# Kernel tuning notes

Hardware: AMD Instinct MI355X
Metric: run time of the kernel (lower is better)

Reference implementation:

```python
import jax, jax.numpy as jnp
import numpy as np

N_NODES = 100000
N_EDGES = 1600000
D_IN, D_HID, D_OUT = 64, 64, 32


def setup_inputs() -> dict:
    key = jax.random.key(0)
    ks = jax.random.split(key, 9)
    x = jax.random.normal(ks[0], (N_NODES, D_IN), dtype=jnp.float32)
    edge_index = jax.random.randint(ks[1], (2, N_EDGES), 0, N_NODES, dtype=jnp.int64)
    s1 = 1.0 / np.sqrt(D_IN)
    s2 = 1.0 / np.sqrt(D_HID)
    return {
        "x": x,
        "edge_index": edge_index,
        # layer 1: lin_l (aggregated neighbors, has bias), lin_r (root, no bias)
        "W1_l": jax.random.uniform(ks[2], (D_IN, D_HID), jnp.float32, -s1, s1),
        "b1": jax.random.uniform(ks[3], (D_HID,), jnp.float32, -s1, s1),
        "W1_r": jax.random.uniform(ks[4], (D_IN, D_HID), jnp.float32, -s1, s1),
        # layer 2
        "W2_l": jax.random.uniform(ks[5], (D_HID, D_OUT), jnp.float32, -s2, s2),
        "b2": jax.random.uniform(ks[6], (D_OUT,), jnp.float32, -s2, s2),
        "W2_r": jax.random.uniform(ks[7], (D_HID, D_OUT), jnp.float32, -s2, s2),
    }


def _sage_conv(x, src, dst, W_l, b_l, W_r, n_nodes):
    """PyG SAGEConv with mean aggregation:
       out_i = W_l @ mean_{j in N(i)} x_j + b_l + W_r @ x_i
    """
    msgs = x[src]  # [E, d] gather of source-node features
    summed = jax.ops.segment_sum(msgs, dst, num_segments=n_nodes)  # [N, d]
    deg = jax.ops.segment_sum(jnp.ones((src.shape[0],), x.dtype), dst, num_segments=n_nodes)
    mean = summed / jnp.maximum(deg, 1.0)[:, None]
    return mean @ W_l + b_l + x @ W_r


def reference(x, edge_index, W1_l, b1, W1_r, W2_l, b2, W2_r):
    src, dst = edge_index[0], edge_index[1]
    n = x.shape[0]
    h = _sage_conv(x, src, dst, W1_l, b1, W1_r, n)
    h = jax.nn.relu(h)
    out = _sage_conv(h, src, dst, W2_l, b2, W2_r, n)
    return out
```

## Files before the change

### kernel.cpp

```cpp
#include <hip/hip_runtime.h>


typedef __attribute__((ext_vector_type(4))) float f4;
typedef __attribute__((ext_vector_type(2))) float f2;
typedef __attribute__((ext_vector_type(4))) unsigned short us4;
typedef __attribute__((ext_vector_type(8))) unsigned short us8;
typedef __attribute__((ext_vector_type(8))) short bfrag;

#define BSHIFT 9
#define BSZ (1 << BSHIFT)
#define NBMAX 256
#define NBLK 512
#define LSTR 72

static __device__ inline unsigned short f2bf(float f) {
    union { float f; unsigned u; } v; v.f = f;
    unsigned u = v.u;
    u = (u + 0x7FFFu + ((u >> 16) & 1u)) >> 16;
    return (unsigned short)u;
}
static __device__ inline float bf2f(unsigned short h) {
    union { unsigned u; float f; } v; v.u = ((unsigned)h) << 16; return v.f;
}

__global__ __launch_bounds__(256) void k_bhist(const int* __restrict__ dst, int E, int chunk,
                                               int NB, int* __restrict__ cntmat) {
    __shared__ int hist[NBMAX];
    int t = threadIdx.x;
    hist[t] = 0;
    __syncthreads();
    int lo = blockIdx.x * chunk, hi = min(lo + chunk, E);
    for (int e = lo + t; e < hi; e += 256) atomicAdd(&hist[dst[e] >> BSHIFT], 1);
    __syncthreads();
    if (t < NB) cntmat[blockIdx.x * NB + t] = hist[t];
}

__global__ __launch_bounds__(256) void k_cscan(int* __restrict__ cntmat, int NB,
                                               int* __restrict__ btot) {
    __shared__ int wt[4];
    int b = blockIdx.x;
    int t = threadIdx.x;
    int v0 = cntmat[(2 * t) * NB + b];
    int v1 = cntmat[(2 * t + 1) * NB + b];
    int tsum = v0 + v1;
    int lane = t & 63, w = t >> 6;
    int p = tsum;
    for (int off = 1; off < 64; off <<= 1) { int u = __shfl_up(p, off); if (lane >= off) p += u; }
    if (lane == 63) wt[w] = p;
    __syncthreads();
    int wb = 0;
    for (int i = 0; i < w; i++) wb += wt[i];
    int excl = wb + p - tsum;
    cntmat[(2 * t) * NB + b] = excl;
    cntmat[(2 * t + 1) * NB + b] = excl + v0;
    if (t == 255) btot[b] = wb + p;
}

__global__ __launch_bounds__(256) void k_bscan(const int* __restrict__ btot, int NB, int E, int N,
                                               int* __restrict__ bucket_base,
                                               int* __restrict__ row_off) {
    __shared__ int wt[4];
    int t = threadIdx.x;
    int v = (t < NB) ? btot[t] : 0;
    int lane = t & 63, w = t >> 6;
    int p = v;
    for (int off = 1; off < 64; off <<= 1) { int u = __shfl_up(p, off); if (lane >= off) p += u; }
    if (lane == 63) wt[w] = p;
    __syncthreads();
    int wb = 0;
    for (int i = 0; i < w; i++) wb += wt[i];
    int incl = wb + p;
    int excl = incl - v;
    if (t < NB) bucket_base[t] = excl;
    if (t == NB - 1) bucket_base[NB] = incl;
    if (t == 0) row_off[N] = E;
}

__global__ __launch_bounds__(256) void k_bscatter(const int* __restrict__ src, const int* __restrict__ dst,
                                                  int E, int chunk, int NB,
                                                  const int* __restrict__ bucket_base,
                                                  const int* __restrict__ cntmat,
                                                  unsigned int* __restrict__ bdata) {
    __shared__ int lbase[NBMAX], lcur[NBMAX];
    int t = threadIdx.x;
    if (t < NB) { lbase[t] = bucket_base[t] + cntmat[blockIdx.x * NB + t]; lcur[t] = 0; }
    __syncthreads();
    int lo = blockIdx.x * chunk, hi = min(lo + chunk, E);
    for (int e = lo + t; e < hi; e += 256) {
        int d = dst[e];
        int b = d >> BSHIFT;
        int pos = lbase[b] + atomicAdd(&lcur[b], 1);
        bdata[pos] = ((unsigned)(d & (BSZ - 1)) << 17) | (unsigned)src[e];
    }
}

__global__ __launch_bounds__(256) void k_bucket_csr(const unsigned int* __restrict__ bdata,
                                                    const int* __restrict__ bucket_base,
                                                    int N, int* __restrict__ row_off,
                                                    int* __restrict__ col_src) {
    __shared__ int fh[BSZ];
    __shared__ int wtot[4];
    int t = threadIdx.x;
    int b = blockIdx.x;
    int ebase = bucket_base[b], eend = bucket_base[b + 1];
    fh[2 * t] = 0; fh[2 * t + 1] = 0;
    __syncthreads();
    for (int i = ebase + t; i < eend; i += 256) atomicAdd(&fh[bdata[i] >> 17], 1);
    __syncthreads();
    int a0 = fh[2 * t], a1 = fh[2 * t + 1];
    int psum = a0 + a1;
    int lane = t & 63, w = t >> 6;
    int v = psum;
    for (int off = 1; off < 64; off <<= 1) { int u = __shfl_up(v, off); if (lane >= off) v += u; }
    if (lane == 63) wtot[w] = v;
    __syncthreads();
    int wbase = 0;
    for (int i = 0; i < w; i++) wbase += wtot[i];
    int excl = wbase + v - psum;
    int e0 = excl, e1 = excl + a0;
    int n0 = (b << BSHIFT) + 2 * t, n1 = n0 + 1;
    if (n0 < N) row_off[n0] = ebase + e0;
    if (n1 < N) row_off[n1] = ebase + e1;
    fh[2 * t] = e0; fh[2 * t + 1] = e1;
    __syncthreads();
    for (int i = ebase + t; i < eend; i += 256) {
        unsigned vv = bdata[i];
        int dl = vv >> 17;
        int pos = atomicAdd(&fh[dl], 1);
        col_src[ebase + pos] = (int)(vv & 0x1FFFFu);
    }
}

__global__ __launch_bounds__(256) void k_gemm1(const float* __restrict__ x,
                                               const float* __restrict__ Wl,
                                               const float* __restrict__ Wr, int N,
                                               unsigned char* __restrict__ t1l8,
                                               float* __restrict__ t1r) {
    __shared__ unsigned short sX[64 * LSTR];
    __shared__ unsigned short sW[128 * LSTR];
    int t = threadIdx.x;
    int r0 = blockIdx.x * 64;
    for (int i = t; i < 2048; i += 256) {
        int which = i >> 10;
        int rem = i & 1023;
        int k = rem >> 4;
        int c4 = (rem & 15) * 4;
        f4 v = *(const f4*)&(which ? Wr : Wl)[k * 64 + c4];
        int nb = which * 64 + c4;
        sW[(nb + 0) * LSTR + k] = f2bf(v[0]);
        sW[(nb + 1) * LSTR + k] = f2bf(v[1]);
        sW[(nb + 2) * LSTR + k] = f2bf(v[2]);
        sW[(nb + 3) * LSTR + k] = f2bf(v[3]);
    }
    {
        int row = t >> 2;
        int q = (t & 3) * 16;
        bool valid = (r0 + row) < N;
#pragma unroll
        for (int j = 0; j < 4; j++) {
            f4 v = {0.f, 0.f, 0.f, 0.f};
            if (valid) v = *(const f4*)&x[(size_t)(r0 + row) * 64 + q + j * 4];
            us4 bv;
            bv[0] = f2bf(v[0]); bv[1] = f2bf(v[1]); bv[2] = f2bf(v[2]); bv[3] = f2bf(v[3]);
            *(us4*)&sX[row * LSTR + q + j * 4] = bv;
        }
    }
    __syncthreads();
    int wv = t >> 6;
    int l  = t & 63;
    int lm = l & 15;
    int lk = (l >> 4) * 8;
    f4 acc[8] = {{0.f,0.f,0.f,0.f},{0.f,0.f,0.f,0.f},{0.f,0.f,0.f,0.f},{0.f,0.f,0.f,0.f},
                 {0.f,0.f,0.f,0.f},{0.f,0.f,0.f,0.f},{0.f,0.f,0.f,0.f},{0.f,0.f,0.f,0.f}};
#pragma unroll
    for (int kh = 0; kh < 2; kh++) {
        bfrag a = *(const bfrag*)&sX[(wv * 16 + lm) * LSTR + kh * 32 + lk];
#pragma unroll
        for (int nt = 0; nt < 8; nt++) {
            bfrag b = *(const bfrag*)&sW[(nt * 16 + lm) * LSTR + kh * 32 + lk];
            acc[nt] = __builtin_amdgcn_mfma_f32_16x16x32_bf16(a, b, acc[nt], 0, 0, 0);
        }
    }
    int orow0 = r0 + wv * 16 + (l >> 4) * 4;
#pragma unroll
    for (int j = 0; j < 4; j++) {
        int rr = orow0 + j;
        if (rr < N) {
#pragma unroll
            for (int nt = 0; nt < 4; nt++) {
                float v = acc[nt][j];
                unsigned w8 = __builtin_amdgcn_cvt_pk_fp8_f32(v, v, 0u, false);
                t1l8[(size_t)rr * 64 + nt * 16 + lm] = (unsigned char)(w8 & 0xFFu);
            }
#pragma unroll
            for (int nt = 0; nt < 4; nt++) {
                t1r[(size_t)rr * 64 + nt * 16 + lm] = acc[nt + 4][j];
            }
        }
    }
}

__global__ __launch_bounds__(256) void k_gemm2(const unsigned short* __restrict__ hbf,
                                               const float* __restrict__ Wl,
                                               const float* __restrict__ Wr,
                                               const float* __restrict__ b2, int N,
                                               unsigned short* __restrict__ t2l,
                                               float* __restrict__ t2r) {
    __shared__ unsigned short sX[64 * LSTR];
    __shared__ unsigned short sW[64 * LSTR];
    int t = threadIdx.x;
    int r0 = blockIdx.x * 64;
    for (int i = t; i < 1024; i += 256) {
        int which = i >> 9;
        int rem = i & 511;
        int k = rem >> 3;
        int c4 = (rem & 7) * 4;
        f4 v = *(const f4*)&(which ? Wr : Wl)[k * 32 + c4];
        int nb = which * 32 + c4;
        sW[(nb + 0) * LSTR + k] = f2bf(v[0]);
        sW[(nb + 1) * LSTR + k] = f2bf(v[1]);
        sW[(nb + 2) * LSTR + k] = f2bf(v[2]);
        sW[(nb + 3) * LSTR + k] = f2bf(v[3]);
    }
    {
        int row = t >> 2;
        int q = (t & 3) * 16;
        us8 z = {0,0,0,0,0,0,0,0};
        us8 v0 = z, v1 = z;
        if (r0 + row < N) {
            v0 = *(const us8*)&hbf[(size_t)(r0 + row) * 64 + q];
            v1 = *(const us8*)&hbf[(size_t)(r0 + row) * 64 + q + 8];
        }
        *(us8*)&sX[row * LSTR + q] = v0;
        *(us8*)&sX[row * LSTR + q + 8] = v1;
    }
    __syncthreads();
    int wv = t >> 6;
    int l  = t & 63;
    int lm = l & 15;
    int lk = (l >> 4) * 8;
    f4 acc[4] = {{0.f,0.f,0.f,0.f},{0.f,0.f,0.f,0.f},{0.f,0.f,0.f,0.f},{0.f,0.f,0.f,0.f}};
#pragma unroll
    for (int kh = 0; kh < 2; kh++) {
        bfrag a = *(const bfrag*)&sX[(wv * 16 + lm) * LSTR + kh * 32 + lk];
#pragma unroll
        for (int nt = 0; nt < 4; nt++) {
            bfrag b = *(const bfrag*)&sW[(nt * 16 + lm) * LSTR + kh * 32 + lk];
            acc[nt] = __builtin_amdgcn_mfma_f32_16x16x32_bf16(a, b, acc[nt], 0, 0, 0);
        }
    }
    int orow0 = r0 + wv * 16 + (l >> 4) * 4;
#pragma unroll
    for (int j = 0; j < 4; j++) {
        int rr = orow0 + j;
        if (rr < N) {
#pragma unroll
            for (int nt = 0; nt < 2; nt++) {
                t2l[(size_t)rr * 32 + nt * 16 + lm] = f2bf(acc[nt][j]);
            }
#pragma unroll
            for (int nt = 0; nt < 2; nt++) {
                int c = nt * 16 + lm;
                t2r[(size_t)rr * 32 + c] = acc[nt + 2][j] + b2[c];
            }
        }
    }
}

__global__ __launch_bounds__(256) void k_agg1(const unsigned char* __restrict__ t1l8,
                                              const int* __restrict__ row_off,
                                              const int* __restrict__ col_src,
                                              const float* __restrict__ b1,
                                              const float* __restrict__ t1r,
                                              int N, unsigned short* __restrict__ hbf) {
    int gid = (blockIdx.x * blockDim.x + threadIdx.x) >> 4;
    int gl  = threadIdx.x & 15;
    if (gid >= N) return;
    int beg = row_off[gid], end = row_off[gid + 1];
    f4 a0 = {0.f,0.f,0.f,0.f}, a1 = {0.f,0.f,0.f,0.f};
    f4 a2 = {0.f,0.f,0.f,0.f}, a3 = {0.f,0.f,0.f,0.f};
    int k = beg;
    for (; k + 3 < end; k += 4) {
        int i0 = col_src[k], i1 = col_src[k + 1], i2 = col_src[k + 2], i3 = col_src[k + 3];
        unsigned u0 = *(const unsigned*)&t1l8[(size_t)i0 * 64 + gl * 4];
        unsigned u1 = *(const unsigned*)&t1l8[(size_t)i1 * 64 + gl * 4];
        unsigned u2 = *(const unsigned*)&t1l8[(size_t)i2 * 64 + gl * 4];
        unsigned u3 = *(const unsigned*)&t1l8[(size_t)i3 * 64 + gl * 4];
        f2 l0 = __builtin_amdgcn_cvt_pk_f32_fp8(u0, false), h0 = __builtin_amdgcn_cvt_pk_f32_fp8(u0, true);
        f2 l1 = __builtin_amdgcn_cvt_pk_f32_fp8(u1, false), h1 = __builtin_amdgcn_cvt_pk_f32_fp8(u1, true);
        f2 l2 = __builtin_amdgcn_cvt_pk_f32_fp8(u2, false), h2 = __builtin_amdgcn_cvt_pk_f32_fp8(u2, true);
        f2 l3 = __builtin_amdgcn_cvt_pk_f32_fp8(u3, false), h3 = __builtin_amdgcn_cvt_pk_f32_fp8(u3, true);
        a0[0] += l0[0]; a0[1] += l0[1]; a0[2] += h0[0]; a0[3] += h0[1];
        a1[0] += l1[0]; a1[1] += l1[1]; a1[2] += h1[0]; a1[3] += h1[1];
        a2[0] += l2[0]; a2[1] += l2[1]; a2[2] += h2[0]; a2[3] += h2[1];
        a3[0] += l3[0]; a3[1] += l3[1]; a3[2] += h3[0]; a3[3] += h3[1];
    }
    for (; k < end; k++) {
        unsigned u0 = *(const unsigned*)&t1l8[(size_t)col_src[k] * 64 + gl * 4];
        f2 l0 = __builtin_amdgcn_cvt_pk_f32_fp8(u0, false), h0 = __builtin_amdgcn_cvt_pk_f32_fp8(u0, true);
        a0[0] += l0[0]; a0[1] += l0[1]; a0[2] += h0[0]; a0[3] += h0[1];
    }
    f4 s = (a0 + a1) + (a2 + a3);
    float deg = (float)(end - beg);
    float inv = deg > 0.f ? 1.f / deg : 0.f;
    f4 rr = *(const f4*)&t1r[(size_t)gid * 64 + gl * 4];
    f4 bb = *(const f4*)&b1[gl * 4];
    us4 ob;
#pragma unroll
    for (int j = 0; j < 4; j++) {
        float v = s[j] * inv + rr[j] + bb[j];
        ob[j] = f2bf(v > 0.f ? v : 0.f);
    }
    *(us4*)&hbf[(size_t)gid * 64 + gl * 4] = ob;
}

__global__ __launch_bounds__(256) void k_agg2(const unsigned short* __restrict__ t2l,
                                              const float* __restrict__ t2r,
                                              const int* __restrict__ row_off,
                                              const int* __restrict__ col_src,
                                              int N, float* __restrict__ out) {
    int gid = (blockIdx.x * blockDim.x + threadIdx.x) >> 4;
    int gl  = threadIdx.x & 15;
    if (gid >= N) return;
    int beg = row_off[gid], end = row_off[gid + 1];
    f2 a0 = {0.f,0.f}, a1 = {0.f,0.f}, a2 = {0.f,0.f}, a3 = {0.f,0.f};
    int k = beg;
    for (; k + 3 < end; k += 4) {
        int i0 = col_src[k], i1 = col_src[k + 1], i2 = col_src[k + 2], i3 = col_src[k + 3];
        unsigned u0 = *(const unsigned*)&t2l[(size_t)i0 * 32 + gl * 2];
        unsigned u1 = *(const unsigned*)&t2l[(size_t)i1 * 32 + gl * 2];
        unsigned u2 = *(const unsigned*)&t2l[(size_t)i2 * 32 + gl * 2];
        unsigned u3 = *(const unsigned*)&t2l[(size_t)i3 * 32 + gl * 2];
        a0[0] += bf2f((unsigned short)(u0 & 0xFFFFu)); a0[1] += bf2f((unsigned short)(u0 >> 16));
        a1[0] += bf2f((unsigned short)(u1 & 0xFFFFu)); a1[1] += bf2f((unsigned short)(u1 >> 16));
        a2[0] += bf2f((unsigned short)(u2 & 0xFFFFu)); a2[1] += bf2f((unsigned short)(u2 >> 16));
        a3[0] += bf2f((unsigned short)(u3 & 0xFFFFu)); a3[1] += bf2f((unsigned short)(u3 >> 16));
    }
    for (; k < end; k++) {
        unsigned u0 = *(const unsigned*)&t2l[(size_t)col_src[k] * 32 + gl * 2];
        a0[0] += bf2f((unsigned short)(u0 & 0xFFFFu)); a0[1] += bf2f((unsigned short)(u0 >> 16));
    }
    f2 s = (a0 + a1) + (a2 + a3);
    float deg = (float)(end - beg);
    float inv = deg > 0.f ? 1.f / deg : 0.f;
    f2 rr = *(const f2*)&t2r[(size_t)gid * 32 + gl * 2];
    f2 o = {s[0] * inv + rr[0], s[1] * inv + rr[1]};
    *(f2*)&out[(size_t)gid * 32 + gl * 2] = o;
}

extern "C" void kernel_launch(void* const* d_in, const int* in_sizes, int n_in,
                              void* d_out, int out_size, void* d_ws, size_t ws_size,
                              hipStream_t stream) {
    const float* x   = (const float*)d_in[0];
    const int*   ei  = (const int*)d_in[1];
    const float* W1l = (const float*)d_in[2];
    const float* b1  = (const float*)d_in[3];
    const float* W1r = (const float*)d_in[4];
    const float* W2l = (const float*)d_in[5];
    const float* b2  = (const float*)d_in[6];
    const float* W2r = (const float*)d_in[7];
    float* out = (float*)d_out;

    int N = in_sizes[0] / 64;
    int E = in_sizes[1] / 2;
    const int* src = ei;
    const int* dst = ei + E;
    int NB = (N + BSZ - 1) >> BSHIFT;

    char* ws = (char*)d_ws;
    size_t off = 0;
    auto alloc = [&](size_t bytes) { void* p = ws + off; off += (bytes + 255) & ~(size_t)255; return p; };
    int* cntmat      = (int*)alloc((size_t)NBLK * NB * 4);
    int* btot        = (int*)alloc((size_t)NB * 4);
    int* bucket_base = (int*)alloc((size_t)(NB + 1) * 4);
    int* row_off     = (int*)alloc((size_t)(N + 1) * 4);
    int* col_src     = (int*)alloc((size_t)E * 4);
    unsigned int* bdata = (unsigned int*)alloc((size_t)E * 4);
    unsigned char* t1l8 = (unsigned char*)alloc((size_t)N * 64);
    float* t1r          = (float*)alloc((size_t)N * 64 * 4);
    unsigned short* hbf = (unsigned short*)alloc((size_t)N * 64 * 2);

    unsigned short* t2l = (unsigned short*)bdata;
    float* t2r          = t1r;

    int chunk = (E + NBLK - 1) / NBLK;
    k_bhist<<<NBLK, 256, 0, stream>>>(dst, E, chunk, NB, cntmat);
    k_cscan<<<NB, 256, 0, stream>>>(cntmat, NB, btot);
    k_bscan<<<1, 256, 0, stream>>>(btot, NB, E, N, bucket_base, row_off);
    k_bscatter<<<NBLK, 256, 0, stream>>>(src, dst, E, chunk, NB, bucket_base, cntmat, bdata);
    k_bucket_csr<<<NB, 256, 0, stream>>>(bdata, bucket_base, N, row_off, col_src);

    int gb = (N + 63) / 64;
    k_gemm1<<<gb, 256, 0, stream>>>(x, W1l, W1r, N, t1l8, t1r);
    k_agg1<<<((size_t)N * 16 + 255) / 256, 256, 0, stream>>>(t1l8, row_off, col_src, b1, t1r, N, hbf);
    k_gemm2<<<gb, 256, 0, stream>>>(hbf, W2l, W2r, b2, N, t2l, t2r);
    k_agg2<<<((size_t)N * 16 + 255) / 256, 256, 0, stream>>>(t2l, t2r, row_off, col_src, N, out);
}
```

Before: 142.2 us.

## Split gather tables into feature planes, fold bucket scan, store root term bf16

The gathered neighbor tables for both layers are split into two column planes: layer 1 fp8 as 32-byte rows, layer 2 bf16 as 32-byte rows. Each aggregation kernel is launched twice, once per plane, so each pass gathers from a table half the size and is more likely to stay cache-resident. The single-block bucket scan kernel is removed; its prefix sum is recomputed redundantly inside the scatter and CSR kernels, saving one launch. The layer-1 root term is stored as bf16 instead of fp32, halving that traffic at some precision cost, but the CSR indices and row offsets are now read twice per layer.

```diff
diff --git a/kernel.cpp b/kernel.cpp
--- a/kernel.cpp
+++ b/kernel.cpp
@@ -35,8 +35,8 @@
     if (t < NB) cntmat[blockIdx.x * NB + t] = hist[t];
 }
 
-__global__ __launch_bounds__(256) void k_cscan(int* __restrict__ cntmat, int NB,
-                                               int* __restrict__ btot) {
+__global__ __launch_bounds__(256) void k_cscan(int* __restrict__ cntmat, int NB, int E, int N,
+                                               int* __restrict__ btot, int* __restrict__ row_off) {
     __shared__ int wt[4];
     int b = blockIdx.x;
     int t = threadIdx.x;
@@ -54,11 +54,15 @@
     cntmat[(2 * t) * NB + b] = excl;
     cntmat[(2 * t + 1) * NB + b] = excl + v0;
     if (t == 255) btot[b] = wb + p;
-}
-
-__global__ __launch_bounds__(256) void k_bscan(const int* __restrict__ btot, int NB, int E, int N,
-                                               int* __restrict__ bucket_base,
-                                               int* __restrict__ row_off) {
+    if (b == 0 && t == 0) row_off[N] = E;
+}
+
+__global__ __launch_bounds__(256) void k_bscatter(const int* __restrict__ src, const int* __restrict__ dst,
+                                                  int E, int chunk, int NB,
+                                                  const int* __restrict__ btot,
+                                                  const int* __restrict__ cntmat,
+                                                  unsigned int* __restrict__ bdata) {
+    __shared__ int lbase[NBMAX], lcur[NBMAX];
     __shared__ int wt[4];
     int t = threadIdx.x;
     int v = (t < NB) ? btot[t] : 0;
@@ -69,21 +73,8 @@
     __syncthreads();
     int wb = 0;
     for (int i = 0; i < w; i++) wb += wt[i];
-    int incl = wb + p;
-    int excl = incl - v;
-    if (t < NB) bucket_base[t] = excl;
-    if (t == NB - 1) bucket_base[NB] = incl;
-    if (t == 0) row_off[N] = E;
-}
-
-__global__ __launch_bounds__(256) void k_bscatter(const int* __restrict__ src, const int* __restrict__ dst,
-                                                  int E, int chunk, int NB,
-                                                  const int* __restrict__ bucket_base,
-                                                  const int* __restrict__ cntmat,
-                                                  unsigned int* __restrict__ bdata) {
-    __shared__ int lbase[NBMAX], lcur[NBMAX];
-    int t = threadIdx.x;
-    if (t < NB) { lbase[t] = bucket_base[t] + cntmat[blockIdx.x * NB + t]; lcur[t] = 0; }
+    int excl = wb + p - v;
+    if (t < NB) { lbase[t] = excl + cntmat[blockIdx.x * NB + t]; lcur[t] = 0; }
     __syncthreads();
     int lo = blockIdx.x * chunk, hi = min(lo + chunk, E);
     for (int e = lo + t; e < hi; e += 256) {
@@ -95,16 +86,29 @@
 }
 
 __global__ __launch_bounds__(256) void k_bucket_csr(const unsigned int* __restrict__ bdata,
-                                                    const int* __restrict__ bucket_base,
+                                                    const int* __restrict__ btot, int NB,
                                                     int N, int* __restrict__ row_off,
                                                     int* __restrict__ col_src) {
     __shared__ int fh[BSZ];
-    __shared__ int wtot[4];
+    __shared__ int wt1[4], wt2[4];
+    __shared__ int sb[2];
     int t = threadIdx.x;
     int b = blockIdx.x;
-    int ebase = bucket_base[b], eend = bucket_base[b + 1];
+    {
+        int v = (t < NB) ? btot[t] : 0;
+        int lane = t & 63, w = t >> 6;
+        int p = v;
+        for (int off = 1; off < 64; off <<= 1) { int u = __shfl_up(p, off); if (lane >= off) p += u; }
+        if (lane == 63) wt1[w] = p;
+        __syncthreads();
+        int wb = 0;
+        for (int i = 0; i < w; i++) wb += wt1[i];
+        int excl = wb + p - v;
+        if (t == b) { sb[0] = excl; sb[1] = excl + v; }
+    }
     fh[2 * t] = 0; fh[2 * t + 1] = 0;
     __syncthreads();
+    int ebase = sb[0], eend = sb[1];
     for (int i = ebase + t; i < eend; i += 256) atomicAdd(&fh[bdata[i] >> 17], 1);
     __syncthreads();
     int a0 = fh[2 * t], a1 = fh[2 * t + 1];
@@ -112,10 +116,10 @@
     int lane = t & 63, w = t >> 6;
     int v = psum;
     for (int off = 1; off < 64; off <<= 1) { int u = __shfl_up(v, off); if (lane >= off) v += u; }
-    if (lane == 63) wtot[w] = v;
+    if (lane == 63) wt2[w] = v;
     __syncthreads();
     int wbase = 0;
-    for (int i = 0; i < w; i++) wbase += wtot[i];
+    for (int i = 0; i < w; i++) wbase += wt2[i];
     int excl = wbase + v - psum;
     int e0 = excl, e1 = excl + a0;
     int n0 = (b << BSHIFT) + 2 * t, n1 = n0 + 1;
@@ -135,7 +139,7 @@
                                                const float* __restrict__ Wl,
                                                const float* __restrict__ Wr, int N,
                                                unsigned char* __restrict__ t1l8,
-                                               float* __restrict__ t1r) {
+                                               unsigned short* __restrict__ t1rb) {
     __shared__ unsigned short sX[64 * LSTR];
     __shared__ unsigned short sW[128 * LSTR];
     int t = threadIdx.x;
@@ -181,6 +185,7 @@
             acc[nt] = __builtin_amdgcn_mfma_f32_16x16x32_bf16(a, b, acc[nt], 0, 0, 0);
         }
     }
+    size_t plane_sz = (size_t)N * 32;
     int orow0 = r0 + wv * 16 + (l >> 4) * 4;
 #pragma unroll
     for (int j = 0; j < 4; j++) {
@@ -190,11 +195,12 @@
             for (int nt = 0; nt < 4; nt++) {
                 float v = acc[nt][j];
                 unsigned w8 = __builtin_amdgcn_cvt_pk_fp8_f32(v, v, 0u, false);
-                t1l8[(size_t)rr * 64 + nt * 16 + lm] = (unsigned char)(w8 & 0xFFu);
+                t1l8[(nt >> 1) * plane_sz + (size_t)rr * 32 + (nt & 1) * 16 + lm] =
+                    (unsigned char)(w8 & 0xFFu);
             }
 #pragma unroll
             for (int nt = 0; nt < 4; nt++) {
-                t1r[(size_t)rr * 64 + nt * 16 + lm] = acc[nt + 4][j];
+                t1rb[(size_t)rr * 64 + nt * 16 + lm] = f2bf(acc[nt + 4][j]);
             }
         }
     }
@@ -249,6 +255,7 @@
             acc[nt] = __builtin_amdgcn_mfma_f32_16x16x32_bf16(a, b, acc[nt], 0, 0, 0);
         }
     }
+    size_t plane_sz = (size_t)N * 16;
     int orow0 = r0 + wv * 16 + (l >> 4) * 4;
 #pragma unroll
     for (int j = 0; j < 4; j++) {
@@ -256,7 +263,7 @@
         if (rr < N) {
 #pragma unroll
             for (int nt = 0; nt < 2; nt++) {
-                t2l[(size_t)rr * 32 + nt * 16 + lm] = f2bf(acc[nt][j]);
+                t2l[nt * plane_sz + (size_t)rr * 16 + lm] = f2bf(acc[nt][j]);
             }
 #pragma unroll
             for (int nt = 0; nt < 2; nt++) {
@@ -267,14 +274,15 @@
     }
 }
 
-__global__ __launch_bounds__(256) void k_agg1(const unsigned char* __restrict__ t1l8,
+__global__ __launch_bounds__(256) void k_agg1(const unsigned char* __restrict__ plane,
                                               const int* __restrict__ row_off,
                                               const int* __restrict__ col_src,
                                               const float* __restrict__ b1,
-                                              const float* __restrict__ t1r,
-                                              int N, unsigned short* __restrict__ hbf) {
-    int gid = (blockIdx.x * blockDim.x + threadIdx.x) >> 4;
-    int gl  = threadIdx.x & 15;
+                                              const unsigned short* __restrict__ t1rb,
+                                              int N, int dimoff,
+                                              unsigned short* __restrict__ hbf) {
+    int gid = (blockIdx.x * blockDim.x + threadIdx.x) >> 3;
+    int gl  = threadIdx.x & 7;
     if (gid >= N) return;
     int beg = row_off[gid], end = row_off[gid + 1];
     f4 a0 = {0.f,0.f,0.f,0.f}, a1 = {0.f,0.f,0.f,0.f};
@@ -282,10 +290,10 @@
     int k = beg;
     for (; k + 3 < end; k += 4) {
         int i0 = col_src[k], i1 = col_src[k + 1], i2 = col_src[k + 2], i3 = col_src[k + 3];
-        unsigned u0 = *(const unsigned*)&t1l8[(size_t)i0 * 64 + gl * 4];
-        unsigned u1 = *(const unsigned*)&t1l8[(size_t)i1 * 64 + gl * 4];
-        unsigned u2 = *(const unsigned*)&t1l8[(size_t)i2 * 64 + gl * 4];
-        unsigned u3 = *(const unsigned*)&t1l8[(size_t)i3 * 64 + gl * 4];
+        unsigned u0 = *(const unsigned*)&plane[(size_t)i0 * 32 + gl * 4];
+        unsigned u1 = *(const unsigned*)&plane[(size_t)i1 * 32 + gl * 4];
+        unsigned u2 = *(const unsigned*)&plane[(size_t)i2 * 32 + gl * 4];
+        unsigned u3 = *(const unsigned*)&plane[(size_t)i3 * 32 + gl * 4];
         f2 l0 = __builtin_amdgcn_cvt_pk_f32_fp8(u0, false), h0 = __builtin_amdgcn_cvt_pk_f32_fp8(u0, true);
         f2 l1 = __builtin_amdgcn_cvt_pk_f32_fp8(u1, false), h1 = __builtin_amdgcn_cvt_pk_f32_fp8(u1, true);
         f2 l2 = __builtin_amdgcn_cvt_pk_f32_fp8(u2, false), h2 = __builtin_amdgcn_cvt_pk_f32_fp8(u2, true);
@@ -296,56 +304,56 @@
         a3[0] += l3[0]; a3[1] += l3[1]; a3[2] += h3[0]; a3[3] += h3[1];
     }
     for (; k < end; k++) {
-        unsigned u0 = *(const unsigned*)&t1l8[(size_t)col_src[k] * 64 + gl * 4];
+        unsigned u0 = *(const unsigned*)&plane[(size_t)col_src[k] * 32 + gl * 4];
         f2 l0 = __builtin_amdgcn_cvt_pk_f32_fp8(u0, false), h0 = __builtin_amdgcn_cvt_pk_f32_fp8(u0, true);
         a0[0] += l0[0]; a0[1] += l0[1]; a0[2] += h0[0]; a0[3] += h0[1];
     }
     f4 s = (a0 + a1) + (a2 + a3);
     float deg = (float)(end - beg);
     float inv = deg > 0.f ? 1.f / deg : 0.f;
-    f4 rr = *(const f4*)&t1r[(size_t)gid * 64 + gl * 4];
-    f4 bb = *(const f4*)&b1[gl * 4];
+    us4 rb = *(const us4*)&t1rb[(size_t)gid * 64 + dimoff + gl * 4];
+    f4 bb = *(const f4*)&b1[dimoff + gl * 4];
     us4 ob;
 #pragma unroll
     for (int j = 0; j < 4; j++) {
-        float v = s[j] * inv + rr[j] + bb[j];
+        float v = s[j] * inv + bf2f(rb[j]) + bb[j];
         ob[j] = f2bf(v > 0.f ? v : 0.f);
     }
-    *(us4*)&hbf[(size_t)gid * 64 + gl * 4] = ob;
-}
-
-__global__ __launch_bounds__(256) void k_agg2(const unsigned short* __restrict__ t2l,
+    *(us4*)&hbf[(size_t)gid * 64 + dimoff + gl * 4] = ob;
+}
+
+__global__ __launch_bounds__(256) void k_agg2(const unsigned short* __restrict__ plane,
                                               const float* __restrict__ t2r,
                                               const int* __restrict__ row_off,
                                               const int* __restrict__ col_src,
-                                              int N, float* __restrict__ out) {
-    int gid = (blockIdx.x * blockDim.x + threadIdx.x) >> 4;
-    int gl  = threadIdx.x & 15;
+                                              int N, int dimoff, float* __restrict__ out) {
+    int gid = (blockIdx.x * blockDim.x + threadIdx.x) >> 3;
+    int gl  = threadIdx.x & 7;
     if (gid >= N) return;
     int beg = row_off[gid], end = row_off[gid + 1];
     f2 a0 = {0.f,0.f}, a1 = {0.f,0.f}, a2 = {0.f,0.f}, a3 = {0.f,0.f};
     int k = beg;
     for (; k + 3 < end; k += 4) {
         int i0 = col_src[k], i1 = col_src[k + 1], i2 = col_src[k + 2], i3 = col_src[k + 3];
-        unsigned u0 = *(const unsigned*)&t2l[(size_t)i0 * 32 + gl * 2];
-        unsigned u1 = *(const unsigned*)&t2l[(size_t)i1 * 32 + gl * 2];
-        unsigned u2 = *(const unsigned*)&t2l[(size_t)i2 * 32 + gl * 2];
-        unsigned u3 = *(const unsigned*)&t2l[(size_t)i3 * 32 + gl * 2];
+        unsigned u0 = *(const unsigned*)&plane[(size_t)i0 * 16 + gl * 2];
+        unsigned u1 = *(const unsigned*)&plane[(size_t)i1 * 16 + gl * 2];
+        unsigned u2 = *(const unsigned*)&plane[(size_t)i2 * 16 + gl * 2];
+        unsigned u3 = *(const unsigned*)&plane[(size_t)i3 * 16 + gl * 2];
         a0[0] += bf2f((unsigned short)(u0 & 0xFFFFu)); a0[1] += bf2f((unsigned short)(u0 >> 16));
         a1[0] += bf2f((unsigned short)(u1 & 0xFFFFu)); a1[1] += bf2f((unsigned short)(u1 >> 16));
         a2[0] += bf2f((unsigned short)(u2 & 0xFFFFu)); a2[1] += bf2f((unsigned short)(u2 >> 16));
         a3[0] += bf2f((unsigned short)(u3 & 0xFFFFu)); a3[1] += bf2f((unsigned short)(u3 >> 16));
     }
     for (; k < end; k++) {
-        unsigned u0 = *(const unsigned*)&t2l[(size_t)col_src[k] * 32 + gl * 2];
+        unsigned u0 = *(const unsigned*)&plane[(size_t)col_src[k] * 16 + gl * 2];
         a0[0] += bf2f((unsigned short)(u0 & 0xFFFFu)); a0[1] += bf2f((unsigned short)(u0 >> 16));
     }
     f2 s = (a0 + a1) + (a2 + a3);
     float deg = (float)(end - beg);
     float inv = deg > 0.f ? 1.f / deg : 0.f;
-    f2 rr = *(const f2*)&t2r[(size_t)gid * 32 + gl * 2];
+    f2 rr = *(const f2*)&t2r[(size_t)gid * 32 + dimoff + gl * 2];
     f2 o = {s[0] * inv + rr[0], s[1] * inv + rr[1]};
-    *(f2*)&out[(size_t)gid * 32 + gl * 2] = o;
+    *(f2*)&out[(size_t)gid * 32 + dimoff + gl * 2] = o;
 }
 
 extern "C" void kernel_launch(void* const* d_in, const int* in_sizes, int n_in,
@@ -372,27 +380,28 @@
     auto alloc = [&](size_t bytes) { void* p = ws + off; off += (bytes + 255) & ~(size_t)255; return p; };
     int* cntmat      = (int*)alloc((size_t)NBLK * NB * 4);
     int* btot        = (int*)alloc((size_t)NB * 4);
-    int* bucket_base = (int*)alloc((size_t)(NB + 1) * 4);
     int* row_off     = (int*)alloc((size_t)(N + 1) * 4);
     int* col_src     = (int*)alloc((size_t)E * 4);
     unsigned int* bdata = (unsigned int*)alloc((size_t)E * 4);
     unsigned char* t1l8 = (unsigned char*)alloc((size_t)N * 64);
-    float* t1r          = (float*)alloc((size_t)N * 64 * 4);
-    unsigned short* hbf = (unsigned short*)alloc((size_t)N * 64 * 2);
+    unsigned short* t1rb = (unsigned short*)alloc((size_t)N * 64 * 2);
+    unsigned short* hbf  = (unsigned short*)alloc((size_t)N * 64 * 2);
 
     unsigned short* t2l = (unsigned short*)bdata;
-    float* t2r          = t1r;
+    float* t2r          = (float*)t1rb;
 
     int chunk = (E + NBLK - 1) / NBLK;
     k_bhist<<<NBLK, 256, 0, stream>>>(dst, E, chunk, NB, cntmat);
-    k_cscan<<<NB, 256, 0, stream>>>(cntmat, NB, btot);
-    k_bscan<<<1, 256, 0, stream>>>(btot, NB, E, N, bucket_base, row_off);
-    k_bscatter<<<NBLK, 256, 0, stream>>>(src, dst, E, chunk, NB, bucket_base, cntmat, bdata);
-    k_bucket_csr<<<NB, 256, 0, stream>>>(bdata, bucket_base, N, row_off, col_src);
+    k_cscan<<<NB, 256, 0, stream>>>(cntmat, NB, E, N, btot, row_off);
+    k_bscatter<<<NBLK, 256, 0, stream>>>(src, dst, E, chunk, NB, btot, cntmat, bdata);
+    k_bucket_csr<<<NB, 256, 0, stream>>>(bdata, btot, NB, N, row_off, col_src);
 
     int gb = (N + 63) / 64;
-    k_gemm1<<<gb, 256, 0, stream>>>(x, W1l, W1r, N, t1l8, t1r);
-    k_agg1<<<((size_t)N * 16 + 255) / 256, 256, 0, stream>>>(t1l8, row_off, col_src, b1, t1r, N, hbf);
+    int ab = ((size_t)N * 8 + 255) / 256;
+    k_gemm1<<<gb, 256, 0, stream>>>(x, W1l, W1r, N, t1l8, t1rb);
+    k_agg1<<<ab, 256, 0, stream>>>(t1l8,                    row_off, col_src, b1, t1rb, N, 0,  hbf);
+    k_agg1<<<ab, 256, 0, stream>>>(t1l8 + (size_t)N * 32,   row_off, col_src, b1, t1rb, N, 32, hbf);
     k_gemm2<<<gb, 256, 0, stream>>>(hbf, W2l, W2r, b2, N, t2l, t2r);
-    k_agg2<<<((size_t)N * 16 + 255) / 256, 256, 0, stream>>>(t2l, t2r, row_off, col_src, N, out);
-}
+    k_agg2<<<ab, 256, 0, stream>>>(t2l,                   t2r, row_off, col_src, N, 0,  out);
+    k_agg2<<<ab, 256, 0, stream>>>(t2l + (size_t)N * 16,  t2r, row_off, col_src, N, 16, out);
+}
```

Result: slower. 159.0 us (+11.8%).
